# Kernel tuning notes

Hardware: AMD Instinct MI355X
Metric: run time of the kernel (lower is better)

The kernel has to match this reference:

```python
import jax, jax.numpy as jnp
import numpy as np

D_MODEL = 1024
N_HEADS = 16


def setup_inputs() -> dict:
    key = jax.random.key(0)
    ks = jax.random.split(key, 5)
    B, L, D = 2, 2048, D_MODEL
    x = jax.random.normal(ks[0], (B, L, D), dtype=jnp.float32)
    # Linear params (torch nn.Linear: y = x @ W.T + b); store as (in, out) for einsum.
    s_attn = 1.0 / np.sqrt(D)
    W_attn = jax.random.uniform(ks[1], (D, 3 * D), jnp.float32, -s_attn, s_attn)
    b_attn = jax.random.uniform(ks[2], (3 * D,), jnp.float32, -s_attn, s_attn)
    W_proj = jax.random.uniform(ks[3], (D, D), jnp.float32, -s_attn, s_attn)
    b_proj = jax.random.uniform(ks[4], (D,), jnp.float32, -s_attn, s_attn)
    return {"x": x, "W_attn": W_attn, "b_attn": b_attn, "W_proj": W_proj, "b_proj": b_proj}


def reference(x, W_attn, b_attn, W_proj, b_proj):
    B, L, D = x.shape
    H = N_HEADS
    hd = D // H
    qkv = jnp.einsum('bld,de->ble', x, W_attn) + b_attn  # [B,L,3D]
    # Faithful to source bug: q and v are both taken from the k projection.
    k_lin = qkv[:, :, D:2 * D]
    k = k_lin.reshape(B, L, H, hd).transpose(0, 2, 1, 3)  # [B,H,L,hd]
    q = k
    v = k
    att = jnp.einsum('bhqd,bhkd->bhqk', q, k) / jnp.sqrt(jnp.float32(hd))
    att = jax.nn.softmax(att, axis=3)
    out = jnp.einsum('bhqk,bhkd->bhqd', att, v)  # [B,H,L,hd]
    out = out.transpose(0, 2, 1, 3).reshape(B, L, D)
    return jnp.einsum('bld,de->ble', out, W_proj) + b_proj
```

## Files before the change

### kernel.cpp

```cpp
#include <hip/hip_runtime.h>
#include <hip/hip_bf16.h>

typedef __attribute__((ext_vector_type(8))) short short8;
typedef __attribute__((ext_vector_type(4))) float f32x4;
typedef __attribute__((ext_vector_type(16))) float f32x16;
typedef unsigned short u16;
typedef unsigned int u32;

static __device__ __forceinline__ u16 f2b(float f) {
  __hip_bfloat16 h = __float2bfloat16(f);
  return __builtin_bit_cast(u16, h);
}
static __device__ __forceinline__ float b2f(u16 v) {
  return __builtin_bit_cast(float, ((u32)v) << 16);
}
static __device__ __forceinline__ u32 pk2(float lo, float hi) {
  return (u32)f2b(lo) | ((u32)f2b(hi) << 16);
}
static __device__ __forceinline__ u32 cvtpk(float lo, float hi) {
  u32 r;
  asm("v_cvt_pk_bf16_f32 %0, %1, %2" : "=v"(r) : "v"(lo), "v"(hi));
  return r;
}

static __device__ __forceinline__ void gload16(const void* g, void* l) {
  __builtin_amdgcn_global_load_lds((const __attribute__((address_space(1))) void*)g,
                                   (__attribute__((address_space(3))) void*)l, 16, 0, 0);
}

static __device__ __forceinline__ void barrier_fenced() {
  __builtin_amdgcn_sched_barrier(0);
  asm volatile("" ::: "memory");
  __builtin_amdgcn_s_barrier();
  __builtin_amdgcn_sched_barrier(0);
  asm volatile("" ::: "memory");
}

__global__ __launch_bounds__(256) void prep(const float4* __restrict__ x4,
                                            uint2* __restrict__ xb,
                                            const float* __restrict__ W_attn,
                                            u16* __restrict__ Wkt,
                                            const float* __restrict__ W_proj,
                                            u16* __restrict__ Wpt) {
  __shared__ u16 tile[32][33];
  int bid = blockIdx.x, t = threadIdx.x;
  if (bid < 4096) {
    int i = bid * 256 + t;
    float4 v = x4[i];
    uint2 o;
    o.x = pk2(v.x, v.y);
    o.y = pk2(v.z, v.w);
    xb[i] = o;
    return;
  }
  const float* in;
  u16* out;
  int in_rs, col_off, blk;
  if (bid < 5120) {
    in = W_attn; out = Wkt; in_rs = 3072; col_off = 1024; blk = bid - 4096;
  } else {
    in = W_proj; out = Wpt; in_rs = 1024; col_off = 0; blk = bid - 5120;
  }
  int tx = t & 31, ty = t >> 5;
  int r0 = (blk >> 5) * 32, c0 = (blk & 31) * 32;
#pragma unroll
  for (int i = 0; i < 4; ++i) {
    int r = r0 + ty + i * 8;
    tile[ty + i * 8][tx] = f2b(in[(size_t)r * in_rs + col_off + c0 + tx]);
  }
  __syncthreads();
#pragma unroll
  for (int i = 0; i < 4; ++i) {
    int c = c0 + ty + i * 8;
    out[(size_t)c * 1024 + r0 + tx] = tile[tx][ty + i * 8];
  }
}

template <int MODE>
__global__ __launch_bounds__(256) void gemm_bias(const u16* __restrict__ A,
                                                 const u16* __restrict__ Bt,
                                                 const float* __restrict__ bias,
                                                 void* __restrict__ Cp, u16* __restrict__ Ktp,
                                                 int M, int N, int K) {
  __shared__ char lds[2][16384];
  int tid = threadIdx.x, lane = tid & 63, wid = tid >> 6;
  int lr = lane & 15, lh = lane >> 4;
  int rb = blockIdx.x;
  int bid = (rb & 7) * 128 + (rb >> 3);
  int m0 = (bid >> 4) << 6, n0 = (bid & 15) << 6;
  int wm = wid >> 1, wn = wid & 1;
  f32x4 acc[2][2] = {};
  int srow = lane >> 3;
  int scol = ((lane & 7) << 4) ^ (srow << 4);
  const char* Ab = (const char*)A;
  const char* Bb = (const char*)Bt;
  const int NT = K >> 6;

  auto stage = [&](char* buf, int k0) {
    char* lA = buf;
    char* lB = buf + 8192;
#pragma unroll
    for (int j = 0; j < 2; ++j) {
      int rg = wid * 16 + j * 8;
      gload16(Ab + ((size_t)(m0 + rg + srow) * K + k0) * 2 + scol, lA + rg * 128);
      gload16(Bb + ((size_t)(n0 + rg + srow) * K + k0) * 2 + scol, lB + rg * 128);
    }
  };

  stage(lds[0], 0);
  for (int t = 0; t < NT; ++t) {
    asm volatile("s_waitcnt vmcnt(0) lgkmcnt(0)" ::: "memory");
    barrier_fenced();
    if (t + 1 < NT) stage(lds[(t + 1) & 1], (t + 1) << 6);
    char* lA = lds[t & 1];
    char* lB = lA + 8192;
    short8 af[2][2], bfr[2][2];
#pragma unroll
    for (int mi = 0; mi < 2; ++mi)
#pragma unroll
      for (int ks = 0; ks < 2; ++ks) {
        int row = wm * 32 + mi * 16 + lr;
        af[mi][ks] = *(const short8*)(lA + row * 128 + ((ks * 64 + lh * 16) ^ ((row & 7) << 4)));
      }
#pragma unroll
    for (int ni = 0; ni < 2; ++ni)
#pragma unroll
      for (int ks = 0; ks < 2; ++ks) {
        int row = wn * 32 + ni * 16 + lr;
        bfr[ni][ks] = *(const short8*)(lB + row * 128 + ((ks * 64 + lh * 16) ^ ((row & 7) << 4)));
      }
    __builtin_amdgcn_s_setprio(1);
#pragma unroll
    for (int ks = 0; ks < 2; ++ks)
#pragma unroll
      for (int mi = 0; mi < 2; ++mi)
#pragma unroll
        for (int ni = 0; ni < 2; ++ni)
          acc[mi][ni] = __builtin_amdgcn_mfma_f32_16x16x32_bf16(af[mi][ks], bfr[ni][ks],
                                                                acc[mi][ni], 0, 0, 0);
    __builtin_amdgcn_s_setprio(0);
  }
#pragma unroll
  for (int mi = 0; mi < 2; ++mi)
#pragma unroll
    for (int ni = 0; ni < 2; ++ni) {
      int col = n0 + wn * 32 + ni * 16 + lr;
      float bz = bias[col];
      int row0 = m0 + wm * 32 + mi * 16 + lh * 4;
      if (MODE == 1) {
#pragma unroll
        for (int r = 0; r < 4; ++r)
          ((float*)Cp)[(size_t)(row0 + r) * N + col] = acc[mi][ni][r] + bz;
      } else {
        ushort4 q;
        u16* qa = (u16*)&q;
#pragma unroll
        for (int r = 0; r < 4; ++r) {
          u16 v = f2b(acc[mi][ni][r] + bz);
          qa[r] = v;
          ((u16*)Cp)[(size_t)(row0 + r) * N + col] = v;
        }
        *(ushort4*)(Ktp + ((size_t)((row0 >> 11) * 1024 + col)) * 2048 + (row0 & 2047)) = q;
      }
    }
}

__global__ __launch_bounds__(256) void flash_attn(const u16* __restrict__ Kb,
                                                  const u16* __restrict__ Kt,
                                                  u16* __restrict__ AO) {
  __shared__ char kv[2][32768];
  const float S2 = 0.125f * 1.44269504088896340736f;
  int tid = threadIdx.x, lane = tid & 63, wid = tid >> 6;
  int ql = lane & 31, half = lane >> 5;
  int rb = blockIdx.x;
  int bid = (rb & 7) * 64 + (rb >> 3);
  int qb = bid & 15, h = (bid >> 4) & 15, b = bid >> 8;
  int qbase = b * 2048 + qb * 128 + wid * 32;
  int hc = h * 64;
  short8 qfr[4];
#pragma unroll
  for (int ds = 0; ds < 4; ++ds) {
    short8 raw = *(const short8*)(Kb + (size_t)(qbase + ql) * 1024 + hc + ds * 16 + half * 8);
    short8 q;
#pragma unroll
    for (int j = 0; j < 8; ++j) q[j] = (short)f2b(b2f((u16)raw[j]) * S2);
    qfr[ds] = q;
  }
  const short8 ones = {0x3F80, 0x3F80, 0x3F80, 0x3F80, 0x3F80, 0x3F80, 0x3F80, 0x3F80};
  f32x16 acc0 = {}, acc1 = {}, accs = {};
  int srow = lane >> 3;
  int scol = ((lane & 7) << 4) ^ (srow << 4);
  const char* Kbase = (const char*)Kb + (size_t)(b * 2048) * 2048 + hc * 2;
  const char* Vbase = (const char*)Kt + (size_t)((b * 16 + h) * 64) * 4096;

  auto stage_pair = [&](char* buf, int pt) {
#pragma unroll
    for (int tt = 0; tt < 2; ++tt) {
      int kt = 2 * pt + tt;
      const char* kp = Kbase + (size_t)(kt * 64) * 2048;
      const char* vp = Vbase + (size_t)(kt * 128);
      char* lk = buf + tt * 16384;
      char* lv = lk + 8192;
#pragma unroll
      for (int j = 0; j < 2; ++j) {
        int row = wid * 8 + j * 32 + srow;
        gload16(kp + (size_t)row * 2048 + scol, lk + (wid * 8 + j * 32) * 128);
        gload16(vp + (size_t)row * 4096 + scol, lv + (wid * 8 + j * 32) * 128);
      }
    }
  };

  auto read_kf = [&](const char* lk, short8 kf[2][4]) {
#pragma unroll
    for (int kb = 0; kb < 2; ++kb)
#pragma unroll
      for (int ds = 0; ds < 4; ++ds) {
        int row = kb * 32 + ql;
        kf[kb][ds] = *(const short8*)(lk + row * 128 + ((ds * 32 + half * 16) ^ ((row & 7) << 4)));
      }
  };
  auto read_vf = [&](const char* lv, short8 vf0[4], short8 vf1[4]) {
#pragma unroll
    for (int ks = 0; ks < 4; ++ks) {
      int row0 = ql, row1 = 32 + ql;
      vf0[ks] = *(const short8*)(lv + row0 * 128 + ((ks * 32 + half * 16) ^ ((row0 & 7) << 4)));
      vf1[ks] = *(const short8*)(lv + row1 * 128 + ((ks * 32 + half * 16) ^ ((row1 & 7) << 4)));
    }
  };
  auto softmax_pack = [&](const f32x16& s0, const f32x16& s1, short8 pa[4]) {
    float p[32];
#pragma unroll
    for (int i = 0; i < 16; ++i) p[i] = __builtin_amdgcn_exp2f(s0[i]);
#pragma unroll
    for (int i = 0; i < 16; ++i) p[16 + i] = __builtin_amdgcn_exp2f(s1[i]);
    u32 w0[8], w1[8];
#pragma unroll
    for (int g = 0; g < 8; ++g) {
      int idx = (g >> 2) * 16 + (g & 3) * 4;
      w0[g] = cvtpk(p[idx], p[idx + 1]);
      w1[g] = cvtpk(p[idx + 2], p[idx + 3]);
    }
#pragma unroll
    for (int ks = 0; ks < 4; ++ks) {
      u32 a0 = w0[2 * ks], b0 = w0[2 * ks + 1];
      u32 a1 = w1[2 * ks], b1 = w1[2 * ks + 1];
      asm volatile("v_permlane32_swap_b32 %0, %1" : "+v"(a0), "+v"(b0));
      asm volatile("v_permlane32_swap_b32 %0, %1" : "+v"(a1), "+v"(b1));
      uint4 words = {a0, a1, b0, b1};
      pa[ks] = __builtin_bit_cast(short8, words);
    }
  };

  stage_pair(kv[0], 0);
  for (int pt = 0; pt < 16; ++pt) {
    asm volatile("s_waitcnt vmcnt(0) lgkmcnt(0)" ::: "memory");
    barrier_fenced();
    if (pt + 1 < 16) stage_pair(kv[(pt + 1) & 1], pt + 1);
    const char* lkA = kv[pt & 1];
    const char* lvA = lkA + 8192;
    const char* lkB = lkA + 16384;
    const char* lvB = lkB + 8192;
    short8 kfA[2][4];
    read_kf(lkA, kfA);
    f32x16 s0 = {}, s1 = {};
    __builtin_amdgcn_s_setprio(1);
#pragma unroll
    for (int ds = 0; ds < 4; ++ds) {
      s0 = __builtin_amdgcn_mfma_f32_32x32x16_bf16(kfA[0][ds], qfr[ds], s0, 0, 0, 0);
      s1 = __builtin_amdgcn_mfma_f32_32x32x16_bf16(kfA[1][ds], qfr[ds], s1, 0, 0, 0);
    }
    __builtin_amdgcn_s_setprio(0);
    short8 vfA0[4], vfA1[4];
    read_vf(lvA, vfA0, vfA1);
    short8 paA[4];
    softmax_pack(s0, s1, paA);
    short8 kfB[2][4];
    read_kf(lkB, kfB);
    __builtin_amdgcn_s_setprio(1);
#pragma unroll
    for (int ks = 0; ks < 4; ++ks) {
      acc0 = __builtin_amdgcn_mfma_f32_32x32x16_bf16(paA[ks], vfA0[ks], acc0, 0, 0, 0);
      acc1 = __builtin_amdgcn_mfma_f32_32x32x16_bf16(paA[ks], vfA1[ks], acc1, 0, 0, 0);
      accs = __builtin_amdgcn_mfma_f32_32x32x16_bf16(paA[ks], ones, accs, 0, 0, 0);
    }
    __builtin_amdgcn_s_setprio(0);
    f32x16 t0 = {}, t1 = {};
    __builtin_amdgcn_s_setprio(1);
#pragma unroll
    for (int ds = 0; ds < 4; ++ds) {
      t0 = __builtin_amdgcn_mfma_f32_32x32x16_bf16(kfB[0][ds], qfr[ds], t0, 0, 0, 0);
      t1 = __builtin_amdgcn_mfma_f32_32x32x16_bf16(kfB[1][ds], qfr[ds], t1, 0, 0, 0);
    }
    __builtin_amdgcn_s_setprio(0);
    short8 vfB0[4], vfB1[4];
    read_vf(lvB, vfB0, vfB1);
    short8 paB[4];
    softmax_pack(t0, t1, paB);
    __builtin_amdgcn_s_setprio(1);
#pragma unroll
    for (int ks = 0; ks < 4; ++ks) {
      acc0 = __builtin_amdgcn_mfma_f32_32x32x16_bf16(paB[ks], vfB0[ks], acc0, 0, 0, 0);
      acc1 = __builtin_amdgcn_mfma_f32_32x32x16_bf16(paB[ks], vfB1[ks], acc1, 0, 0, 0);
      accs = __builtin_amdgcn_mfma_f32_32x32x16_bf16(paB[ks], ones, accs, 0, 0, 0);
    }
    __builtin_amdgcn_s_setprio(0);
  }
#pragma unroll
  for (int reg = 0; reg < 16; ++reg) {
    int ridx = (reg & 3) + 8 * (reg >> 2) + 4 * half;
    float iv = __builtin_amdgcn_rcpf(accs[reg]);
    int grow = qbase + ridx;
    AO[(size_t)grow * 1024 + hc + ql] = f2b(acc0[reg] * iv);
    AO[(size_t)grow * 1024 + hc + 32 + ql] = f2b(acc1[reg] * iv);
  }
}


extern "C" void kernel_launch(void* const* d_in, const int* in_sizes, int n_in, void* d_out,
                              int out_size, void* d_ws, size_t ws_size, hipStream_t stream) {
  const float* x = (const float*)d_in[0];
  const float* W_attn = (const float*)d_in[1];
  const float* b_attn = (const float*)d_in[2];
  const float* W_proj = (const float*)d_in[3];
  const float* b_proj = (const float*)d_in[4];
  float* out = (float*)d_out;
  char* ws = (char*)d_ws;
  u16* xb = (u16*)(ws);
  u16* Kb = (u16*)(ws + 8388608);
  u16* Kt = (u16*)(ws + 16777216);
  u16* Wkt = (u16*)(ws + 25165824);
  u16* Wpt = (u16*)(ws + 27262976);

  prep<<<6144, 256, 0, stream>>>((const float4*)x, (uint2*)xb, W_attn, Wkt, W_proj, Wpt);
  gemm_bias<0><<<1024, 256, 0, stream>>>(xb, Wkt, b_attn + 1024, (void*)Kb, Kt, 4096, 1024, 1024);
  u16* AO = xb;
  flash_attn<<<512, 256, 0, stream>>>(Kb, Kt, AO);
  gemm_bias<1><<<1024, 256, 0, stream>>>(AO, Wpt, b_proj, (void*)out, nullptr, 4096, 1024, 1024);
}
```

Measured before the change: 88.93 us.

## Process two query tiles per wave to reuse K/V fragments in attention

Each wave in the attention kernel now covers 64 query rows (two 32-row tiles) instead of 32, so each block covers 256 queries and the grid is halved. Every K and V fragment read from LDS now feeds MFMAs for both query tiles, cutting LDS reads and global K/V staging per query. The key loop stages one 64-key tile per iteration instead of a pair, which doubles the number of barriers and halves the shared buffer. The cost is more accumulator registers and half as many blocks, which may lower occupancy or leave compute units under-filled.

```diff
diff --git a/kernel.cpp b/kernel.cpp
--- a/kernel.cpp
+++ b/kernel.cpp
@@ -168,65 +168,51 @@
 __global__ __launch_bounds__(256) void flash_attn(const u16* __restrict__ Kb,
                                                   const u16* __restrict__ Kt,
                                                   u16* __restrict__ AO) {
-  __shared__ char kv[2][32768];
+  __shared__ char kv[2][16384];
   const float S2 = 0.125f * 1.44269504088896340736f;
   int tid = threadIdx.x, lane = tid & 63, wid = tid >> 6;
   int ql = lane & 31, half = lane >> 5;
   int rb = blockIdx.x;
-  int bid = (rb & 7) * 64 + (rb >> 3);
-  int qb = bid & 15, h = (bid >> 4) & 15, b = bid >> 8;
-  int qbase = b * 2048 + qb * 128 + wid * 32;
+  int bid = (rb & 7) * 32 + (rb >> 3);
+  int qt = bid & 7, h = (bid >> 3) & 15, b = bid >> 7;
+  int qbase = b * 2048 + qt * 256 + wid * 64;
   int hc = h * 64;
-  short8 qfr[4];
+  short8 qfrA[4], qfrB[4];
 #pragma unroll
   for (int ds = 0; ds < 4; ++ds) {
-    short8 raw = *(const short8*)(Kb + (size_t)(qbase + ql) * 1024 + hc + ds * 16 + half * 8);
-    short8 q;
-#pragma unroll
-    for (int j = 0; j < 8; ++j) q[j] = (short)f2b(b2f((u16)raw[j]) * S2);
-    qfr[ds] = q;
+    short8 rawA = *(const short8*)(Kb + (size_t)(qbase + ql) * 1024 + hc + ds * 16 + half * 8);
+    short8 rawB =
+        *(const short8*)(Kb + (size_t)(qbase + 32 + ql) * 1024 + hc + ds * 16 + half * 8);
+    short8 qa, qb2;
+#pragma unroll
+    for (int j = 0; j < 8; ++j) {
+      qa[j] = (short)f2b(b2f((u16)rawA[j]) * S2);
+      qb2[j] = (short)f2b(b2f((u16)rawB[j]) * S2);
+    }
+    qfrA[ds] = qa;
+    qfrB[ds] = qb2;
   }
   const short8 ones = {0x3F80, 0x3F80, 0x3F80, 0x3F80, 0x3F80, 0x3F80, 0x3F80, 0x3F80};
-  f32x16 acc0 = {}, acc1 = {}, accs = {};
+  f32x16 accA0 = {}, accA1 = {}, accAs = {};
+  f32x16 accB0 = {}, accB1 = {}, accBs = {};
   int srow = lane >> 3;
   int scol = ((lane & 7) << 4) ^ (srow << 4);
   const char* Kbase = (const char*)Kb + (size_t)(b * 2048) * 2048 + hc * 2;
   const char* Vbase = (const char*)Kt + (size_t)((b * 16 + h) * 64) * 4096;
 
-  auto stage_pair = [&](char* buf, int pt) {
-#pragma unroll
-    for (int tt = 0; tt < 2; ++tt) {
-      int kt = 2 * pt + tt;
-      const char* kp = Kbase + (size_t)(kt * 64) * 2048;
-      const char* vp = Vbase + (size_t)(kt * 128);
-      char* lk = buf + tt * 16384;
-      char* lv = lk + 8192;
-#pragma unroll
-      for (int j = 0; j < 2; ++j) {
-        int row = wid * 8 + j * 32 + srow;
-        gload16(kp + (size_t)row * 2048 + scol, lk + (wid * 8 + j * 32) * 128);
-        gload16(vp + (size_t)row * 4096 + scol, lv + (wid * 8 + j * 32) * 128);
-      }
+  auto stage = [&](char* buf, int kt) {
+    const char* kp = Kbase + (size_t)(kt * 64) * 2048;
+    const char* vp = Vbase + (size_t)(kt * 128);
+    char* lk = buf;
+    char* lv = buf + 8192;
+#pragma unroll
+    for (int j = 0; j < 2; ++j) {
+      int row = wid * 8 + j * 32 + srow;
+      gload16(kp + (size_t)row * 2048 + scol, lk + (wid * 8 + j * 32) * 128);
+      gload16(vp + (size_t)row * 4096 + scol, lv + (wid * 8 + j * 32) * 128);
     }
   };
 
-  auto read_kf = [&](const char* lk, short8 kf[2][4]) {
-#pragma unroll
-    for (int kb = 0; kb < 2; ++kb)
-#pragma unroll
-      for (int ds = 0; ds < 4; ++ds) {
-        int row = kb * 32 + ql;
-        kf[kb][ds] = *(const short8*)(lk + row * 128 + ((ds * 32 + half * 16) ^ ((row & 7) << 4)));
-      }
-  };
-  auto read_vf = [&](const char* lv, short8 vf0[4], short8 vf1[4]) {
-#pragma unroll
-    for (int ks = 0; ks < 4; ++ks) {
-      int row0 = ql, row1 = 32 + ql;
-      vf0[ks] = *(const short8*)(lv + row0 * 128 + ((ks * 32 + half * 16) ^ ((row0 & 7) << 4)));
-      vf1[ks] = *(const short8*)(lv + row1 * 128 + ((ks * 32 + half * 16) ^ ((row1 & 7) << 4)));
-    }
-  };
   auto softmax_pack = [&](const f32x16& s0, const f32x16& s1, short8 pa[4]) {
     float p[32];
 #pragma unroll
@@ -251,67 +237,64 @@
     }
   };
 
-  stage_pair(kv[0], 0);
-  for (int pt = 0; pt < 16; ++pt) {
+  stage(kv[0], 0);
+  for (int kt = 0; kt < 32; ++kt) {
     asm volatile("s_waitcnt vmcnt(0) lgkmcnt(0)" ::: "memory");
     barrier_fenced();
-    if (pt + 1 < 16) stage_pair(kv[(pt + 1) & 1], pt + 1);
-    const char* lkA = kv[pt & 1];
-    const char* lvA = lkA + 8192;
-    const char* lkB = lkA + 16384;
-    const char* lvB = lkB + 8192;
-    short8 kfA[2][4];
-    read_kf(lkA, kfA);
-    f32x16 s0 = {}, s1 = {};
+    if (kt + 1 < 32) stage(kv[(kt + 1) & 1], kt + 1);
+    const char* lk = kv[kt & 1];
+    const char* lv = lk + 8192;
+    short8 kf[2][4];
+#pragma unroll
+    for (int kb = 0; kb < 2; ++kb)
+#pragma unroll
+      for (int ds = 0; ds < 4; ++ds) {
+        int row = kb * 32 + ql;
+        kf[kb][ds] = *(const short8*)(lk + row * 128 + ((ds * 32 + half * 16) ^ ((row & 7) << 4)));
+      }
+    f32x16 sA0 = {}, sA1 = {}, sB0 = {}, sB1 = {};
     __builtin_amdgcn_s_setprio(1);
 #pragma unroll
     for (int ds = 0; ds < 4; ++ds) {
-      s0 = __builtin_amdgcn_mfma_f32_32x32x16_bf16(kfA[0][ds], qfr[ds], s0, 0, 0, 0);
-      s1 = __builtin_amdgcn_mfma_f32_32x32x16_bf16(kfA[1][ds], qfr[ds], s1, 0, 0, 0);
+      sA0 = __builtin_amdgcn_mfma_f32_32x32x16_bf16(kf[0][ds], qfrA[ds], sA0, 0, 0, 0);
+      sB0 = __builtin_amdgcn_mfma_f32_32x32x16_bf16(kf[0][ds], qfrB[ds], sB0, 0, 0, 0);
+      sA1 = __builtin_amdgcn_mfma_f32_32x32x16_bf16(kf[1][ds], qfrA[ds], sA1, 0, 0, 0);
+      sB1 = __builtin_amdgcn_mfma_f32_32x32x16_bf16(kf[1][ds], qfrB[ds], sB1, 0, 0, 0);
     }
     __builtin_amdgcn_s_setprio(0);
-    short8 vfA0[4], vfA1[4];
-    read_vf(lvA, vfA0, vfA1);
-    short8 paA[4];
-    softmax_pack(s0, s1, paA);
-    short8 kfB[2][4];
-    read_kf(lkB, kfB);
+    short8 paA[4], paB[4];
+    softmax_pack(sA0, sA1, paA);
+    softmax_pack(sB0, sB1, paB);
+    short8 vf0[4], vf1[4];
+#pragma unroll
+    for (int ks = 0; ks < 4; ++ks) {
+      int row0 = ql, row1 = 32 + ql;
+      vf0[ks] = *(const short8*)(lv + row0 * 128 + ((ks * 32 + half * 16) ^ ((row0 & 7) << 4)));
+      vf1[ks] = *(const short8*)(lv + row1 * 128 + ((ks * 32 + half * 16) ^ ((row1 & 7) << 4)));
+    }
     __builtin_amdgcn_s_setprio(1);
 #pragma unroll
     for (int ks = 0; ks < 4; ++ks) {
-      acc0 = __builtin_amdgcn_mfma_f32_32x32x16_bf16(paA[ks], vfA0[ks], acc0, 0, 0, 0);
-      acc1 = __builtin_amdgcn_mfma_f32_32x32x16_bf16(paA[ks], vfA1[ks], acc1, 0, 0, 0);
-      accs = __builtin_amdgcn_mfma_f32_32x32x16_bf16(paA[ks], ones, accs, 0, 0, 0);
-    }
-    __builtin_amdgcn_s_setprio(0);
-    f32x16 t0 = {}, t1 = {};
-    __builtin_amdgcn_s_setprio(1);
-#pragma unroll
-    for (int ds = 0; ds < 4; ++ds) {
-      t0 = __builtin_amdgcn_mfma_f32_32x32x16_bf16(kfB[0][ds], qfr[ds], t0, 0, 0, 0);
-      t1 = __builtin_amdgcn_mfma_f32_32x32x16_bf16(kfB[1][ds], qfr[ds], t1, 0, 0, 0);
-    }
-    __builtin_amdgcn_s_setprio(0);
-    short8 vfB0[4], vfB1[4];
-    read_vf(lvB, vfB0, vfB1);
-    short8 paB[4];
-    softmax_pack(t0, t1, paB);
-    __builtin_amdgcn_s_setprio(1);
-#pragma unroll
-    for (int ks = 0; ks < 4; ++ks) {
-      acc0 = __builtin_amdgcn_mfma_f32_32x32x16_bf16(paB[ks], vfB0[ks], acc0, 0, 0, 0);
-      acc1 = __builtin_amdgcn_mfma_f32_32x32x16_bf16(paB[ks], vfB1[ks], acc1, 0, 0, 0);
-      accs = __builtin_amdgcn_mfma_f32_32x32x16_bf16(paB[ks], ones, accs, 0, 0, 0);
+      accA0 = __builtin_amdgcn_mfma_f32_32x32x16_bf16(paA[ks], vf0[ks], accA0, 0, 0, 0);
+      accB0 = __builtin_amdgcn_mfma_f32_32x32x16_bf16(paB[ks], vf0[ks], accB0, 0, 0, 0);
+      accA1 = __builtin_amdgcn_mfma_f32_32x32x16_bf16(paA[ks], vf1[ks], accA1, 0, 0, 0);
+      accB1 = __builtin_amdgcn_mfma_f32_32x32x16_bf16(paB[ks], vf1[ks], accB1, 0, 0, 0);
+      accAs = __builtin_amdgcn_mfma_f32_32x32x16_bf16(paA[ks], ones, accAs, 0, 0, 0);
+      accBs = __builtin_amdgcn_mfma_f32_32x32x16_bf16(paB[ks], ones, accBs, 0, 0, 0);
     }
     __builtin_amdgcn_s_setprio(0);
   }
 #pragma unroll
   for (int reg = 0; reg < 16; ++reg) {
     int ridx = (reg & 3) + 8 * (reg >> 2) + 4 * half;
-    float iv = __builtin_amdgcn_rcpf(accs[reg]);
-    int grow = qbase + ridx;
-    AO[(size_t)grow * 1024 + hc + ql] = f2b(acc0[reg] * iv);
-    AO[(size_t)grow * 1024 + hc + 32 + ql] = f2b(acc1[reg] * iv);
+    int growA = qbase + ridx;
+    int growB = qbase + 32 + ridx;
+    float ivA = __builtin_amdgcn_rcpf(accAs[reg]);
+    float ivB = __builtin_amdgcn_rcpf(accBs[reg]);
+    AO[(size_t)growA * 1024 + hc + ql] = f2b(accA0[reg] * ivA);
+    AO[(size_t)growA * 1024 + hc + 32 + ql] = f2b(accA1[reg] * ivA);
+    AO[(size_t)growB * 1024 + hc + ql] = f2b(accB0[reg] * ivB);
+    AO[(size_t)growB * 1024 + hc + 32 + ql] = f2b(accB1[reg] * ivB);
   }
 }
 
@@ -334,6 +317,6 @@
   prep<<<6144, 256, 0, stream>>>((const float4*)x, (uint2*)xb, W_attn, Wkt, W_proj, Wpt);
   gemm_bias<0><<<1024, 256, 0, stream>>>(xb, Wkt, b_attn + 1024, (void*)Kb, Kt, 4096, 1024, 1024);
   u16* AO = xb;
-  flash_attn<<<512, 256, 0, stream>>>(Kb, Kt, AO);
+  flash_attn<<<256, 256, 0, stream>>>(Kb, Kt, AO);
   gemm_bias<1><<<1024, 256, 0, stream>>>(AO, Wpt, b_proj, (void*)out, nullptr, 4096, 1024, 1024);
 }
```

Result: slower. 98.18 us (+10.4%).
